# Performance work log

Hardware: AMD Instinct MI355X
Metric: run time of the kernel (lower is better)

## Reference

```python
import jax, jax.numpy as jnp
import numpy as np

TAU = 0.1
EPS_NORM = 1e-12  # torch F.normalize clamp
EPS_DEN = 1e-6


def setup_inputs() -> dict:
    key = jax.random.key(0)
    k1, k2, k3, k4 = jax.random.split(key, 4)
    B, C, H, W = 4, 128, 64, 64
    feat_A = jax.random.normal(k1, (B, C, H, W), dtype=jnp.float32)
    feat_B = jax.random.normal(k2, (B, C, H, W), dtype=jnp.float32)
    H_mat = jax.random.normal(k3, (B, 3, 3), dtype=jnp.float32)
    valid_mask = jax.random.uniform(k4, (B, H, W), dtype=jnp.float32)
    return {"feat_A": feat_A, "feat_B": feat_B, "H_mat": H_mat, "valid_mask": valid_mask}


def _l2_normalize(x, axis):
    n = jnp.sqrt(jnp.sum(x * x, axis=axis, keepdims=True))
    return x / jnp.maximum(n, EPS_NORM)


def reference(feat_A, feat_B, H_mat, valid_mask):
    B, C, H, W = feat_A.shape
    HW = H * W
    fA = _l2_normalize(feat_A.reshape(B, C, HW), axis=1)  # [B, C, HW]
    fB = _l2_normalize(feat_B.reshape(B, C, HW), axis=1)  # [B, C, HW]
    # sim[b, n, m] = <fA[:, :, n], fB[:, :, m]> / tau
    sim = jnp.einsum('bcn,bcm->bnm', fA, fB) / TAU  # [B, HW, HW]
    # torch CE with input [B, HW, HW], labels arange(HW): class axis is 1,
    # so logits for position k are the column sim[b, :, k], target = k.
    lse = jax.nn.logsumexp(sim, axis=1)               # [B, HW] (over class axis)
    diag = jnp.einsum('bkk->bk', sim)                 # sim[b, k, k]
    loss = lse - diag                                  # [B, HW], per-position CE
    mask_flat = valid_mask.reshape(B, HW)
    return (loss * mask_flat).sum() / (mask_flat.sum() + EPS_DEN)
```

## Files before the change

### kernel.cpp

```cpp
#include <hip/hip_runtime.h>
#include <math.h>

#define BB 4
#define CC 128
#define HW 4096
#define SC10 3.16227766016838f

typedef short short8 __attribute__((ext_vector_type(8)));
typedef float f32x4 __attribute__((ext_vector_type(4)));

static __device__ inline unsigned short f2bf(float f) {
  unsigned int u = __float_as_uint(f);
  u += 0x7fffu + ((u >> 16) & 1u);
  return (unsigned short)(u >> 16);
}

__global__ __launch_bounds__(256) void k_prep(const float* __restrict__ fA,
                                              const float* __restrict__ fB,
                                              unsigned short* __restrict__ fAn,
                                              unsigned short* __restrict__ fBn,
                                              float* __restrict__ diag,
                                              float* __restrict__ expsum) {
  __shared__ float sA[32 * 129];
  __shared__ float sB[32 * 129];
  __shared__ float red[3 * 256];

  const int bid = blockIdx.x;
  const int b   = bid >> 7;
  const int n0  = (bid & 127) * 32;
  const int tid = threadIdx.x;
  const int cR  = tid >> 5;
  const int n   = tid & 31;

  const float* pa = fA + (size_t)b * CC * HW + n0 + n;
  const float* pb = fB + (size_t)b * CC * HW + n0 + n;

  float ssa = 0.f, ssb = 0.f, dot = 0.f;
  #pragma unroll
  for (int it = 0; it < 16; ++it) {
    int c = it * 8 + cR;
    float va = pa[(size_t)c * HW];
    float vb = pb[(size_t)c * HW];
    sA[n * 129 + c] = va;
    sB[n * 129 + c] = vb;
    ssa = fmaf(va, va, ssa);
    ssb = fmaf(vb, vb, ssb);
    dot = fmaf(va, vb, dot);
  }
  red[tid] = ssa; red[256 + tid] = ssb; red[512 + tid] = dot;
  __syncthreads();

  if (tid < 32) {
    float sa = 0.f, sb = 0.f, dt = 0.f;
    #pragma unroll
    for (int k = 0; k < 8; ++k) {
      sa += red[k * 32 + tid];
      sb += red[256 + k * 32 + tid];
      dt += red[512 + k * 32 + tid];
    }
    float ia = 1.f / fmaxf(sqrtf(sa), 1e-12f);
    float ib = 1.f / fmaxf(sqrtf(sb), 1e-12f);
    int gidx = b * HW + n0 + tid;
    diag[gidx]   = dt * ia * ib * 10.f;
    expsum[gidx] = 0.f;
    red[tid]      = ia * SC10;
    red[32 + tid] = ib * SC10;
  }
  __syncthreads();

  #pragma unroll
  for (int r = 0; r < 2; ++r) {
    int L  = r * 256 + tid;
    int nn = L >> 4;
    int q  = L & 15;
    int c0 = (q ^ (nn & 7)) * 8;
    size_t base = ((size_t)b * HW + n0 + nn) * 128 + q * 8;
    {
      float sc = red[nn];
      const float* s = &sA[nn * 129 + c0];
      uint4 v;
      v.x = f2bf(s[0]*sc) | ((unsigned)f2bf(s[1]*sc) << 16);
      v.y = f2bf(s[2]*sc) | ((unsigned)f2bf(s[3]*sc) << 16);
      v.z = f2bf(s[4]*sc) | ((unsigned)f2bf(s[5]*sc) << 16);
      v.w = f2bf(s[6]*sc) | ((unsigned)f2bf(s[7]*sc) << 16);
      *(uint4*)(fAn + base) = v;
    }
    {
      float sc = red[32 + nn];
      const float* s = &sB[nn * 129 + c0];
      uint4 v;
      v.x = f2bf(s[0]*sc) | ((unsigned)f2bf(s[1]*sc) << 16);
      v.y = f2bf(s[2]*sc) | ((unsigned)f2bf(s[3]*sc) << 16);
      v.z = f2bf(s[4]*sc) | ((unsigned)f2bf(s[5]*sc) << 16);
      v.w = f2bf(s[6]*sc) | ((unsigned)f2bf(s[7]*sc) << 16);
      *(uint4*)(fBn + base) = v;
    }
  }
}

__global__ __launch_bounds__(256) void k_main(const unsigned short* __restrict__ fAn,
                                              const unsigned short* __restrict__ fBn,
                                              float* __restrict__ expsum) {
  __shared__ unsigned short sAB[2 * 128 * 128];
  unsigned short* sA = sAB;
  unsigned short* sB = sAB + 16384;

  const int bid = blockIdx.x;
  const int b   = bid >> 10;
  const int tl  = bid & 1023;
  const int n0  = (tl >> 5) * 128;
  const int m0  = (tl & 31) * 128;
  const int tid = threadIdx.x;

  const unsigned short* gA = fAn + ((size_t)b * HW + n0) * 128;
  const unsigned short* gB = fBn + ((size_t)b * HW + m0) * 128;

  #pragma unroll
  for (int r = 0; r < 8; ++r) {
    int L = r * 256 + tid;
    __builtin_amdgcn_global_load_lds(
        (const __attribute__((address_space(1))) unsigned int*)(gA + (size_t)L * 8),
        (__attribute__((address_space(3))) unsigned int*)(sA + L * 8), 16, 0, 0);
    __builtin_amdgcn_global_load_lds(
        (const __attribute__((address_space(1))) unsigned int*)(gB + (size_t)L * 8),
        (__attribute__((address_space(3))) unsigned int*)(sB + L * 8), 16, 0, 0);
  }
  __syncthreads();

  const int wv   = tid >> 6;
  const int lane = tid & 63;
  const int wn   = (wv & 1) * 64;
  const int wm   = (wv >> 1) * 64;
  const int ml   = lane & 15;
  const int g    = lane >> 4;

  f32x4 acc[4][4] = {};

  #pragma unroll
  for (int kc = 0; kc < 4; ++kc) {
    short8 af[4], bf[4];
    int q = kc * 4 + g;
    #pragma unroll
    for (int s = 0; s < 4; ++s) {
      int na = wn + s * 16 + ml;
      af[s] = *(const short8*)(sA + na * 128 + ((q ^ (na & 7)) * 8));
      int nb = wm + s * 16 + ml;
      bf[s] = *(const short8*)(sB + nb * 128 + ((q ^ (nb & 7)) * 8));
    }
    #pragma unroll
    for (int i = 0; i < 4; ++i)
      #pragma unroll
      for (int j = 0; j < 4; ++j)
        acc[i][j] = __builtin_amdgcn_mfma_f32_16x16x32_bf16(af[i], bf[j], acc[i][j], 0, 0, 0);
  }

  __syncthreads();
  float* sCol = (float*)sAB;
  #pragma unroll
  for (int j = 0; j < 4; ++j) {
    float e = 0.f;
    #pragma unroll
    for (int i = 0; i < 4; ++i)
      #pragma unroll
      for (int r = 0; r < 4; ++r)
        e += __expf(acc[i][j][r] - 10.f);
    e += __shfl_xor(e, 16, 64);
    e += __shfl_xor(e, 32, 64);
    if (lane < 16) sCol[wv * 64 + j * 16 + lane] = e;
  }
  __syncthreads();
  if (tid < 128) {
    int m = tid;
    float sum = (m < 64) ? (sCol[m] + sCol[64 + m])
                         : (sCol[128 + (m - 64)] + sCol[192 + (m - 64)]);
    atomicAdd(&expsum[(size_t)b * HW + m0 + m], sum);
  }
}

__global__ __launch_bounds__(1024) void k_loss(const float* __restrict__ diag,
                                               const float* __restrict__ expsum,
                                               const float* __restrict__ mask,
                                               float* __restrict__ out) {
  __shared__ float rn[1024], rd[1024];
  const int tid = threadIdx.x;
  float num = 0.f, den = 0.f;
  for (int i = tid; i < BB * HW; i += 1024) {
    float lse = 10.f + __logf(expsum[i]);
    float mv  = mask[i];
    num = fmaf(mv, lse - diag[i], num);
    den += mv;
  }
  rn[tid] = num; rd[tid] = den;
  __syncthreads();
  for (int s = 512; s > 0; s >>= 1) {
    if (tid < s) { rn[tid] += rn[tid + s]; rd[tid] += rd[tid + s]; }
    __syncthreads();
  }
  if (tid == 0) out[0] = rn[0] / (rd[0] + 1e-6f);
}

extern "C" void kernel_launch(void* const* d_in, const int* in_sizes, int n_in,
                              void* d_out, int out_size, void* d_ws, size_t ws_size,
                              hipStream_t stream) {
  const float* feat_A = (const float*)d_in[0];
  const float* feat_B = (const float*)d_in[1];
  const float* vmask  = (const float*)d_in[3];

  unsigned short* fAn = (unsigned short*)d_ws;
  unsigned short* fBn = fAn + (size_t)BB * HW * CC;
  float* diag   = (float*)(fBn + (size_t)BB * HW * CC);
  float* expsum = diag + BB * HW;
  float* out    = (float*)d_out;

  k_prep<<<512,  256, 0, stream>>>(feat_A, feat_B, fAn, fBn, diag, expsum);
  k_main<<<4096, 256, 0, stream>>>(fAn, fBn, expsum);
  k_loss<<<1,   1024, 0, stream>>>(diag, expsum, vmask, out);
}
```

Before: 106.5 us.

## Make main kernel persistent over n-tiles, fold scale into exp2, parallelize loss

The main kernel now launches 512 blocks. Each block keeps one B tile resident in LDS and loops over eight A tiles, accumulating column exp-sums in registers. Column sums are atomically added once per block instead of once per tile, which cuts global atomics and B reloads. The normalization scale now includes log2(e)/tau, so the exp becomes a raw exp2 with the max-offset subtraction removed. This relies on logits being bounded by the cosine-similarity range so exp2 cannot overflow. The loss reduction is split across 64 blocks, which combine through atomics and a last-block counter. The A-tile load is not double-buffered, so load latency is exposed on every iteration.

```diff
diff --git a/kernel.cpp b/kernel.cpp
--- a/kernel.cpp
+++ b/kernel.cpp
@@ -4,7 +4,7 @@
 #define BB 4
 #define CC 128
 #define HW 4096
-#define SC10 3.16227766016838f
+#define SCF 3.798282565f
 
 typedef short short8 __attribute__((ext_vector_type(8)));
 typedef float f32x4 __attribute__((ext_vector_type(4)));
@@ -13,6 +13,14 @@
   unsigned int u = __float_as_uint(f);
   u += 0x7fffu + ((u >> 16) & 1u);
   return (unsigned short)(u >> 16);
+}
+
+static __device__ inline float fast_exp2(float x) {
+#if __has_builtin(__builtin_amdgcn_exp2f)
+  return __builtin_amdgcn_exp2f(x);
+#else
+  return exp2f(x);
+#endif
 }
 
 __global__ __launch_bounds__(256) void k_prep(const float* __restrict__ fA,
@@ -20,7 +28,8 @@
                                               unsigned short* __restrict__ fAn,
                                               unsigned short* __restrict__ fBn,
                                               float* __restrict__ diag,
-                                              float* __restrict__ expsum) {
+                                              float* __restrict__ expsum,
+                                              float* __restrict__ acc) {
   __shared__ float sA[32 * 129];
   __shared__ float sB[32 * 129];
   __shared__ float red[3 * 256];
@@ -31,6 +40,8 @@
   const int tid = threadIdx.x;
   const int cR  = tid >> 5;
   const int n   = tid & 31;
+
+  if (bid == 0 && tid == 0) { acc[0] = 0.f; acc[1] = 0.f; ((unsigned*)acc)[2] = 0u; }
 
   const float* pa = fA + (size_t)b * CC * HW + n0 + n;
   const float* pb = fB + (size_t)b * CC * HW + n0 + n;
@@ -63,8 +74,8 @@
     int gidx = b * HW + n0 + tid;
     diag[gidx]   = dt * ia * ib * 10.f;
     expsum[gidx] = 0.f;
-    red[tid]      = ia * SC10;
-    red[32 + tid] = ib * SC10;
+    red[tid]      = ia * SCF;
+    red[32 + tid] = ib * SCF;
   }
   __syncthreads();
 
@@ -98,105 +109,123 @@
   }
 }
 
-__global__ __launch_bounds__(256) void k_main(const unsigned short* __restrict__ fAn,
-                                              const unsigned short* __restrict__ fBn,
-                                              float* __restrict__ expsum) {
-  __shared__ unsigned short sAB[2 * 128 * 128];
-  unsigned short* sA = sAB;
-  unsigned short* sB = sAB + 16384;
+__global__ __launch_bounds__(256, 2) void k_main(const unsigned short* __restrict__ fAn,
+                                                 const unsigned short* __restrict__ fBn,
+                                                 float* __restrict__ expsum) {
+  __shared__ unsigned short sB[128 * 128];
+  __shared__ unsigned short sA[128 * 128];
 
   const int bid = blockIdx.x;
-  const int b   = bid >> 10;
-  const int tl  = bid & 1023;
-  const int n0  = (tl >> 5) * 128;
-  const int m0  = (tl & 31) * 128;
+  const int x   = bid & 7;
+  const int t   = bid >> 3;
+  const int b   = x & 3;
+  const int nq  = (x >> 2) | ((t & 1) << 1);
+  const int mt  = t >> 1;
+  const int m0  = mt * 128;
+  const int nbase = nq * 1024;
   const int tid = threadIdx.x;
 
-  const unsigned short* gA = fAn + ((size_t)b * HW + n0) * 128;
   const unsigned short* gB = fBn + ((size_t)b * HW + m0) * 128;
-
   #pragma unroll
   for (int r = 0; r < 8; ++r) {
     int L = r * 256 + tid;
     __builtin_amdgcn_global_load_lds(
-        (const __attribute__((address_space(1))) unsigned int*)(gA + (size_t)L * 8),
-        (__attribute__((address_space(3))) unsigned int*)(sA + L * 8), 16, 0, 0);
-    __builtin_amdgcn_global_load_lds(
         (const __attribute__((address_space(1))) unsigned int*)(gB + (size_t)L * 8),
         (__attribute__((address_space(3))) unsigned int*)(sB + L * 8), 16, 0, 0);
   }
-  __syncthreads();
 
   const int wv   = tid >> 6;
   const int lane = tid & 63;
+  const int ml   = lane & 15;
+  const int g    = lane >> 4;
   const int wn   = (wv & 1) * 64;
   const int wm   = (wv >> 1) * 64;
-  const int ml   = lane & 15;
-  const int g    = lane >> 4;
-
-  f32x4 acc[4][4] = {};
-
-  #pragma unroll
-  for (int kc = 0; kc < 4; ++kc) {
-    short8 af[4], bf[4];
-    int q = kc * 4 + g;
-    #pragma unroll
-    for (int s = 0; s < 4; ++s) {
-      int na = wn + s * 16 + ml;
-      af[s] = *(const short8*)(sA + na * 128 + ((q ^ (na & 7)) * 8));
-      int nb = wm + s * 16 + ml;
-      bf[s] = *(const short8*)(sB + nb * 128 + ((q ^ (nb & 7)) * 8));
-    }
-    #pragma unroll
-    for (int i = 0; i < 4; ++i)
+
+  float colAcc[4] = {0.f, 0.f, 0.f, 0.f};
+
+  for (int it = 0; it < 8; ++it) {
+    __syncthreads();
+    const unsigned short* gA = fAn + ((size_t)b * HW + nbase + it * 128) * 128;
+    #pragma unroll
+    for (int r = 0; r < 8; ++r) {
+      int L = r * 256 + tid;
+      __builtin_amdgcn_global_load_lds(
+          (const __attribute__((address_space(1))) unsigned int*)(gA + (size_t)L * 8),
+          (__attribute__((address_space(3))) unsigned int*)(sA + L * 8), 16, 0, 0);
+    }
+    __syncthreads();
+
+    f32x4 acc[4][4] = {};
+    #pragma unroll
+    for (int kc = 0; kc < 4; ++kc) {
+      short8 af[4], bf[4];
+      int q = kc * 4 + g;
       #pragma unroll
-      for (int j = 0; j < 4; ++j)
-        acc[i][j] = __builtin_amdgcn_mfma_f32_16x16x32_bf16(af[i], bf[j], acc[i][j], 0, 0, 0);
-  }
-
-  __syncthreads();
-  float* sCol = (float*)sAB;
+      for (int s = 0; s < 4; ++s) {
+        int na = wn + s * 16 + ml;
+        af[s] = *(const short8*)(sA + na * 128 + ((q ^ (na & 7)) * 8));
+        int nb = wm + s * 16 + ml;
+        bf[s] = *(const short8*)(sB + nb * 128 + ((q ^ (nb & 7)) * 8));
+      }
+      #pragma unroll
+      for (int i = 0; i < 4; ++i)
+        #pragma unroll
+        for (int j = 0; j < 4; ++j)
+          acc[i][j] = __builtin_amdgcn_mfma_f32_16x16x32_bf16(af[i], bf[j], acc[i][j], 0, 0, 0);
+    }
+    #pragma unroll
+    for (int j = 0; j < 4; ++j) {
+      float e = 0.f;
+      #pragma unroll
+      for (int i = 0; i < 4; ++i)
+        #pragma unroll
+        for (int r = 0; r < 4; ++r)
+          e += fast_exp2(acc[i][j][r]);
+      colAcc[j] += e;
+    }
+  }
+
   #pragma unroll
   for (int j = 0; j < 4; ++j) {
-    float e = 0.f;
-    #pragma unroll
-    for (int i = 0; i < 4; ++i)
-      #pragma unroll
-      for (int r = 0; r < 4; ++r)
-        e += __expf(acc[i][j][r] - 10.f);
+    float e = colAcc[j];
     e += __shfl_xor(e, 16, 64);
     e += __shfl_xor(e, 32, 64);
-    if (lane < 16) sCol[wv * 64 + j * 16 + lane] = e;
-  }
+    if (lane < 16)
+      atomicAdd(&expsum[(size_t)b * HW + m0 + wm + j * 16 + lane], e);
+  }
+}
+
+__global__ __launch_bounds__(256) void k_loss(const float* __restrict__ diag,
+                                              const float* __restrict__ expsum,
+                                              const float* __restrict__ mask,
+                                              float* __restrict__ acc,
+                                              float* __restrict__ out) {
+  __shared__ float rn[4], rd[4];
+  const int i = blockIdx.x * 256 + threadIdx.x;
+  float lse = __logf(expsum[i]);
+  float mv  = mask[i];
+  float num = mv * (lse - diag[i]);
+  #pragma unroll
+  for (int off = 32; off; off >>= 1) {
+    num += __shfl_down(num, off, 64);
+    mv  += __shfl_down(mv,  off, 64);
+  }
+  const int lane = threadIdx.x & 63, wv = threadIdx.x >> 6;
+  if (lane == 0) { rn[wv] = num; rd[wv] = mv; }
   __syncthreads();
-  if (tid < 128) {
-    int m = tid;
-    float sum = (m < 64) ? (sCol[m] + sCol[64 + m])
-                         : (sCol[128 + (m - 64)] + sCol[192 + (m - 64)]);
-    atomicAdd(&expsum[(size_t)b * HW + m0 + m], sum);
-  }
-}
-
-__global__ __launch_bounds__(1024) void k_loss(const float* __restrict__ diag,
-                                               const float* __restrict__ expsum,
-                                               const float* __restrict__ mask,
-                                               float* __restrict__ out) {
-  __shared__ float rn[1024], rd[1024];
-  const int tid = threadIdx.x;
-  float num = 0.f, den = 0.f;
-  for (int i = tid; i < BB * HW; i += 1024) {
-    float lse = 10.f + __logf(expsum[i]);
-    float mv  = mask[i];
-    num = fmaf(mv, lse - diag[i], num);
-    den += mv;
-  }
-  rn[tid] = num; rd[tid] = den;
-  __syncthreads();
-  for (int s = 512; s > 0; s >>= 1) {
-    if (tid < s) { rn[tid] += rn[tid + s]; rd[tid] += rd[tid + s]; }
-    __syncthreads();
-  }
-  if (tid == 0) out[0] = rn[0] / (rd[0] + 1e-6f);
+  if (threadIdx.x == 0) {
+    float n = rn[0] + rn[1] + rn[2] + rn[3];
+    float d = rd[0] + rd[1] + rd[2] + rd[3];
+    atomicAdd(&acc[0], n);
+    atomicAdd(&acc[1], d);
+    __threadfence();
+    unsigned prev = atomicAdd((unsigned*)(acc + 2), 1u);
+    if (prev == 63u) {
+      float fn = atomicAdd(&acc[0], 0.f);
+      float fd = atomicAdd(&acc[1], 0.f);
+      out[0] = fn / (fd + 1e-6f);
+    }
+  }
 }
 
 extern "C" void kernel_launch(void* const* d_in, const int* in_sizes, int n_in,
@@ -210,9 +239,10 @@
   unsigned short* fBn = fAn + (size_t)BB * HW * CC;
   float* diag   = (float*)(fBn + (size_t)BB * HW * CC);
   float* expsum = diag + BB * HW;
+  float* acc    = expsum + BB * HW;
   float* out    = (float*)d_out;
 
-  k_prep<<<512,  256, 0, stream>>>(feat_A, feat_B, fAn, fBn, diag, expsum);
-  k_main<<<4096, 256, 0, stream>>>(fAn, fBn, expsum);
-  k_loss<<<1,   1024, 0, stream>>>(diag, expsum, vmask, out);
-}
+  k_prep<<<512, 256, 0, stream>>>(feat_A, feat_B, fAn, fBn, diag, expsum, acc);
+  k_main<<<512, 256, 0, stream>>>(fAn, fBn, expsum);
+  k_loss<<<64,  256, 0, stream>>>(diag, expsum, vmask, acc, out);
+}
```

Result: faster. 96.60 us (-9.3%).
